# Performance work log

Hardware: AMD Instinct MI355X
Metric: run time of the kernel (lower is better)

Reference implementation:

```python
import jax, jax.numpy as jnp
import numpy as np

VP = 0.4
EP = 0.21

def _c_matrix():
    # Faithfully replicate the original Ci (including its asymmetric rows 2) and invert.
    Ci = np.zeros((6, 6), dtype=np.float64)
    Ci[0, 0] = 1 / EP; Ci[0, 1] = -VP / EP; Ci[0, 2] = -VP / EP
    Ci[1, 0] = -VP / EP; Ci[1, 1] = 1 / EP; Ci[1, 2] = -VP / EP
    Ci[2, 0] = -VP;      Ci[2, 1] = -VP;      Ci[2, 2] = 1 / EP
    Ci[3, 3] = 2 * (1 + VP) / EP
    Ci[4, 4] = 2 * (1 + VP) / EP
    Ci[5, 5] = 2 * (1 + VP) / EP
    return np.linalg.inv(Ci).astype(np.float32)

C_MAT = jnp.asarray(_c_matrix())
N = 12288

def setup_inputs() -> dict:
    key = jax.random.key(0)
    k1, k2, k3 = jax.random.split(key, 3)
    xyz = jax.random.normal(k1, (N, 3), dtype=jnp.float32)
    new_xyz = jax.random.normal(k2, (N, 3), dtype=jnp.float32)
    # ~half the points are 'inside' (gt_sdf < 1e-8)
    gt_sdf = jax.random.uniform(k3, (N,), dtype=jnp.float32) - 0.5
    return {"new_xyz": new_xyz, "xyz": xyz, "gt_sdf": gt_sdf}

def reference(new_xyz, xyz, gt_sdf):
    motion = new_xyz - xyz                      # [N,3]
    inside = gt_sdf < 1e-8                      # [N] bool, selects inside points
    w = new_xyz                                 # warped coordinates (KNN space)
    n = w.shape[0]
    # Brute-force NN among inside points (KDTree k=2, second neighbor == nearest non-self).
    sq = jnp.sum(w * w, axis=1)                 # [N]
    d2 = sq[:, None] + sq[None, :] - 2.0 * (w @ w.T)   # [N,N] squared distances
    BIG = jnp.float32(1e30)
    bad_col = (~inside)[None, :] | jnp.eye(n, dtype=bool)
    d2 = jnp.where(bad_col, BIG, d2)
    nn_idx = jnp.argmin(d2, axis=1)             # nearest inside neighbor (excluding self)
    nn_d = jnp.sqrt(jnp.maximum(jnp.min(d2, axis=1), 0.0))
    # tree_list1 filter: drop rows whose nearest neighbor is a duplicate point
    valid = inside & (nn_d > 1e-8)              # [N]
    dm = motion[nn_idx] - motion                # motion_delta
    dc = w[nn_idx] - w + 1e-8                   # cords_delta (+1e-8 as in original)
    v = valid[:, None]
    dm = jnp.where(v, dm, 0.0)                  # neutralize masked rows (keep shapes static)
    dc = jnp.where(v, dc, 1.0)
    du, dv, dw = dm[:, 0], dm[:, 1], dm[:, 2]
    dx, dy, dz = dc[:, 0], dc[:, 1], dc[:, 2]
    et = jnp.stack([du / dx, dv / dy, dw / dz,
                    (du / dy + dv / dx) / 2,
                    (du / dz + dw / dx) / 2,
                    (dw / dy + dv / dz) / 2], axis=1)   # [N,6] strain tensor
    # diag(et @ C @ et.T) as an O(N) batched quadratic form
    q = jnp.einsum('ni,ij,nj->n', et, C_MAT, et)
    q = jnp.where(valid, q, 0.0)
    n_valid = jnp.sum(valid).astype(jnp.float32)
    return jnp.linalg.norm(q) / n_valid
```

## Files before the change

### kernel.cpp

```cpp
#include <hip/hip_runtime.h>
#include <math.h>
#include <string.h>

#define N 12288
#define TILE 256
#define IB 512
#define NBX (N / IB)
#define NBY (N / TILE)

typedef unsigned long long ull;

struct CMat { float c[6][6]; };

template<int MODE>
__device__ __forceinline__ void nn_inner(
    const float4* __restrict__ tile, int tid,
    float wx0, float wy0, float wz0,
    float wx1, float wy1, float wz1,
    float& best0, int& bk0, float& best1, int& bk1)
{
    #pragma unroll 8
    for (int k = 0; k < TILE; ++k) {
        const float4 b = tile[k];
        const float d0 = fmaf(-2.0f, wx0 * b.x + wy0 * b.y + wz0 * b.z, b.w);
        const float d1 = fmaf(-2.0f, wx1 * b.x + wy1 * b.y + wz1 * b.z, b.w);
        bool ok0 = d0 < best0;
        bool ok1 = d1 < best1;
        if (MODE == 0) ok0 = ok0 && (k != tid);
        if (MODE == 1) ok1 = ok1 && (k != tid);
        if (ok0) { best0 = d0; bk0 = k; }
        if (ok1) { best1 = d1; bk1 = k; }
    }
}

__global__ __launch_bounds__(256) void nn_kernel(
    const float* __restrict__ new_xyz,
    const float* __restrict__ gt_sdf,
    ull* __restrict__ packed)
{
    const int tid = threadIdx.x;
    const int bx = blockIdx.x;
    const int by = blockIdx.y;

    const int i0 = bx * IB + tid;
    const int i1 = i0 + 256;

    const float wx0 = new_xyz[3 * i0 + 0];
    const float wy0 = new_xyz[3 * i0 + 1];
    const float wz0 = new_xyz[3 * i0 + 2];
    const float wx1 = new_xyz[3 * i1 + 0];
    const float wy1 = new_xyz[3 * i1 + 1];
    const float wz1 = new_xyz[3 * i1 + 2];

    __shared__ float4 tile[TILE];
    {
        const int j = by * TILE + tid;
        const float bxp = new_xyz[3 * j + 0];
        const float byp = new_xyz[3 * j + 1];
        const float bzp = new_xyz[3 * j + 2];
        const float sqj = bxp * bxp + byp * byp + bzp * bzp;
        const bool ins = gt_sdf[j] < 1e-8f;
        tile[tid] = make_float4(bxp, byp, bzp, ins ? sqj : 3e30f);
    }
    __syncthreads();

    float best0 = 3.0e38f, best1 = 3.0e38f;
    int bk0 = 0, bk1 = 0;

    if (by == 2 * bx)
        nn_inner<0>(tile, tid, wx0, wy0, wz0, wx1, wy1, wz1, best0, bk0, best1, bk1);
    else if (by == 2 * bx + 1)
        nn_inner<1>(tile, tid, wx0, wy0, wz0, wx1, wy1, wz1, best0, bk0, best1, bk1);
    else
        nn_inner<2>(tile, tid, wx0, wy0, wz0, wx1, wy1, wz1, best0, bk0, best1, bk1);

    const int jbase = by * TILE;

    unsigned kb0 = __float_as_uint(best0);
    kb0 = ((int)kb0 < 0) ? ~kb0 : (kb0 | 0x80000000u);
    packed[(size_t)by * N + i0] =
        ((ull)kb0 << 32) | (ull)(unsigned)(jbase + bk0);

    unsigned kb1 = __float_as_uint(best1);
    kb1 = ((int)kb1 < 0) ? ~kb1 : (kb1 | 0x80000000u);
    packed[(size_t)by * N + i1] =
        ((ull)kb1 << 32) | (ull)(unsigned)(jbase + bk1);
}

__global__ __launch_bounds__(256) void loss_kernel(
    const float* __restrict__ new_xyz,
    const float* __restrict__ xyz,
    const float* __restrict__ gt_sdf,
    const ull* __restrict__ packed,
    double* __restrict__ partial_sum,
    unsigned int* __restrict__ partial_cnt,
    CMat C)
{
    const int tid = threadIdx.x;
    const int i = blockIdx.x * 256 + tid;

    ull best = ~0ull;
    #pragma unroll
    for (int s = 0; s < NBY; ++s) {
        const ull p = packed[(size_t)s * N + i];
        best = (p < best) ? p : best;
    }

    const unsigned kb = (unsigned)(best >> 32);
    const unsigned bits = (kb & 0x80000000u) ? (kb ^ 0x80000000u) : ~kb;
    const float key = __uint_as_float(bits);
    const int nn = (int)(unsigned)(best & 0xffffffffu);

    const float wix = new_xyz[3 * i + 0];
    const float wiy = new_xyz[3 * i + 1];
    const float wiz = new_xyz[3 * i + 2];
    const float sqi = wix * wix + wiy * wiy + wiz * wiz;

    const float d2 = sqi + key;
    const float nnd = sqrtf(fmaxf(d2, 0.0f));
    const bool inside = gt_sdf[i] < 1e-8f;
    const bool valid = inside && (nnd > 1e-8f);

    float q = 0.0f;
    if (valid) {
        const float xix = xyz[3 * i + 0], xiy = xyz[3 * i + 1], xiz = xyz[3 * i + 2];
        const float wnx = new_xyz[3 * nn + 0], wny = new_xyz[3 * nn + 1], wnz = new_xyz[3 * nn + 2];
        const float xnx = xyz[3 * nn + 0],     xny = xyz[3 * nn + 1],     xnz = xyz[3 * nn + 2];

        const float du = (wnx - xnx) - (wix - xix);
        const float dv = (wny - xny) - (wiy - xiy);
        const float dw = (wnz - xnz) - (wiz - xiz);
        const float dx = wnx - wix + 1e-8f;
        const float dy = wny - wiy + 1e-8f;
        const float dz = wnz - wiz + 1e-8f;

        float et[6];
        et[0] = du / dx;
        et[1] = dv / dy;
        et[2] = dw / dz;
        et[3] = (du / dy + dv / dx) * 0.5f;
        et[4] = (du / dz + dw / dx) * 0.5f;
        et[5] = (dw / dy + dv / dz) * 0.5f;

        #pragma unroll
        for (int a = 0; a < 6; ++a) {
            float s = 0.0f;
            #pragma unroll
            for (int b = 0; b < 6; ++b) s += C.c[a][b] * et[b];
            q += et[a] * s;
        }
    }

    double q2 = (double)q * (double)q;
    #pragma unroll
    for (int off = 32; off > 0; off >>= 1)
        q2 += __shfl_down(q2, off, 64);
    const ull vm = __ballot(valid);
    const int lane = tid & 63;
    const int wid = tid >> 6;

    __shared__ double wsum[4];
    __shared__ unsigned wcnt[4];
    if (lane == 0) { wsum[wid] = q2; wcnt[wid] = (unsigned)__popcll(vm); }
    __syncthreads();
    if (tid == 0) {
        double s = wsum[0] + wsum[1] + wsum[2] + wsum[3];
        unsigned c = wcnt[0] + wcnt[1] + wcnt[2] + wcnt[3];
        partial_sum[blockIdx.x] = s;
        partial_cnt[blockIdx.x] = c;
    }
}

__global__ void final_kernel(const double* __restrict__ partial_sum,
                             const unsigned int* __restrict__ partial_cnt,
                             float* __restrict__ out)
{
    const int lane = threadIdx.x;
    double s = (lane < NBY) ? partial_sum[lane] : 0.0;
    double c = (lane < NBY) ? (double)partial_cnt[lane] : 0.0;
    #pragma unroll
    for (int off = 32; off > 0; off >>= 1) {
        s += __shfl_down(s, off, 64);
        c += __shfl_down(c, off, 64);
    }
    if (lane == 0) out[0] = (float)(sqrt(s) / c);
}

static void build_cmat(CMat* M)
{
    const double VP = 0.4, EP = 0.21;
    double A[6][12];
    memset(A, 0, sizeof(A));
    double Ci[6][6];
    memset(Ci, 0, sizeof(Ci));
    Ci[0][0] = 1.0 / EP; Ci[0][1] = -VP / EP; Ci[0][2] = -VP / EP;
    Ci[1][0] = -VP / EP; Ci[1][1] = 1.0 / EP; Ci[1][2] = -VP / EP;
    Ci[2][0] = -VP;      Ci[2][1] = -VP;      Ci[2][2] = 1.0 / EP;
    Ci[3][3] = 2.0 * (1.0 + VP) / EP;
    Ci[4][4] = Ci[3][3];
    Ci[5][5] = Ci[3][3];

    for (int i = 0; i < 6; ++i) {
        for (int j = 0; j < 6; ++j) A[i][j] = Ci[i][j];
        A[i][6 + i] = 1.0;
    }
    for (int col = 0; col < 6; ++col) {
        int piv = col;
        for (int r = col + 1; r < 6; ++r)
            if (fabs(A[r][col]) > fabs(A[piv][col])) piv = r;
        if (piv != col)
            for (int c = 0; c < 12; ++c) { double t = A[col][c]; A[col][c] = A[piv][c]; A[piv][c] = t; }
        const double d = A[col][col];
        for (int c = 0; c < 12; ++c) A[col][c] /= d;
        for (int r = 0; r < 6; ++r) {
            if (r == col) continue;
            const double f = A[r][col];
            if (f == 0.0) continue;
            for (int c = 0; c < 12; ++c) A[r][c] -= f * A[col][c];
        }
    }
    for (int i = 0; i < 6; ++i)
        for (int j = 0; j < 6; ++j)
            M->c[i][j] = (float)A[i][6 + j];
}

extern "C" void kernel_launch(void* const* d_in, const int* in_sizes, int n_in,
                              void* d_out, int out_size, void* d_ws, size_t ws_size,
                              hipStream_t stream)
{
    const float* new_xyz = (const float*)d_in[0];
    const float* xyz     = (const float*)d_in[1];
    const float* gt_sdf  = (const float*)d_in[2];
    float* out = (float*)d_out;

    const size_t packed_bytes = (size_t)NBY * N * sizeof(ull);
    ull* packed = (ull*)d_ws;
    double* partial_sum = (double*)((char*)d_ws + packed_bytes);
    unsigned int* partial_cnt = (unsigned int*)((char*)d_ws + packed_bytes + NBY * sizeof(double));

    CMat C;
    build_cmat(&C);

    nn_kernel<<<dim3(NBX, NBY), TILE, 0, stream>>>(new_xyz, gt_sdf, packed);
    loss_kernel<<<N / 256, 256, 0, stream>>>(new_xyz, xyz, gt_sdf, packed,
                                             partial_sum, partial_cnt, C);
    final_kernel<<<1, 64, 0, stream>>>(partial_sum, partial_cnt, out);
}
```

Measured before the change: 94.89 us.

## Register-block eight queries per thread with packed FP32 distance math

The nearest-neighbour kernel now holds eight query points per thread instead of two. Distances are computed with two-wide float vectors, so the compiler can emit packed FMA instructions, and the candidate tile shrinks to 96 points. Self-exclusion now checks index equality only in tiles that overlap the query range. The aim is to cut the shared-memory loads and instructions per pair. In exchange, the packed intermediate buffer grows to 128 partial rows per point, which means more global writes and a longer reduction in the loss kernel. The final reduction now uses a separate partial count, since that no longer matches the tile count.

```diff
diff --git a/kernel.cpp b/kernel.cpp
--- a/kernel.cpp
+++ b/kernel.cpp
@@ -3,33 +3,48 @@
 #include <string.h>
 
 #define N 12288
-#define TILE 256
-#define IB 512
+#define TILE 96
+#define ACCS 8
+#define IB (256 * ACCS)
 #define NBX (N / IB)
 #define NBY (N / TILE)
 
 typedef unsigned long long ull;
+typedef float v2f __attribute__((ext_vector_type(2)));
 
 struct CMat { float c[6][6]; };
 
-template<int MODE>
+__device__ __forceinline__ void upd(float dv, int k, bool excl,
+                                    float& bd, int& bk)
+{
+    if (!excl && dv < bd) { bd = dv; bk = k; }
+}
+
+template<bool CAREFUL>
 __device__ __forceinline__ void nn_inner(
-    const float4* __restrict__ tile, int tid,
-    float wx0, float wy0, float wz0,
-    float wx1, float wy1, float wz1,
-    float& best0, int& bk0, float& best1, int& bk1)
+    const float4* __restrict__ tile, int jbase, int ibase_t,
+    const v2f* wx, const v2f* wy, const v2f* wz,
+    float* bd, int* bk)
 {
     #pragma unroll 8
     for (int k = 0; k < TILE; ++k) {
         const float4 b = tile[k];
-        const float d0 = fmaf(-2.0f, wx0 * b.x + wy0 * b.y + wz0 * b.z, b.w);
-        const float d1 = fmaf(-2.0f, wx1 * b.x + wy1 * b.y + wz1 * b.z, b.w);
-        bool ok0 = d0 < best0;
-        bool ok1 = d1 < best1;
-        if (MODE == 0) ok0 = ok0 && (k != tid);
-        if (MODE == 1) ok1 = ok1 && (k != tid);
-        if (ok0) { best0 = d0; bk0 = k; }
-        if (ok1) { best1 = d1; bk1 = k; }
+        const int jj = jbase + k;
+        #pragma unroll
+        for (int g = 0; g < ACCS / 2; ++g) {
+            v2f dot = wx[g] * b.x;
+            dot = dot + wy[g] * b.y;
+            dot = dot + wz[g] * b.z;
+            const v2f d = b.w - 2.0f * dot;
+            const int a0 = 2 * g, a1 = 2 * g + 1;
+            bool e0 = false, e1 = false;
+            if (CAREFUL) {
+                e0 = (jj == ibase_t + a0 * 256);
+                e1 = (jj == ibase_t + a1 * 256);
+            }
+            upd(d.x, k, e0, bd[a0], bk[a0]);
+            upd(d.y, k, e1, bd[a1], bk[a1]);
+        }
     }
 }
 
@@ -42,49 +57,50 @@
     const int bx = blockIdx.x;
     const int by = blockIdx.y;
 
-    const int i0 = bx * IB + tid;
-    const int i1 = i0 + 256;
-
-    const float wx0 = new_xyz[3 * i0 + 0];
-    const float wy0 = new_xyz[3 * i0 + 1];
-    const float wz0 = new_xyz[3 * i0 + 2];
-    const float wx1 = new_xyz[3 * i1 + 0];
-    const float wy1 = new_xyz[3 * i1 + 1];
-    const float wz1 = new_xyz[3 * i1 + 2];
+    const int ibase = bx * IB;
+    const int ibase_t = ibase + tid;
+
+    v2f wx[ACCS / 2], wy[ACCS / 2], wz[ACCS / 2];
+    #pragma unroll
+    for (int g = 0; g < ACCS / 2; ++g) {
+        const int ia = ibase_t + (2 * g) * 256;
+        const int ib2 = ibase_t + (2 * g + 1) * 256;
+        wx[g] = (v2f){ new_xyz[3 * ia + 0], new_xyz[3 * ib2 + 0] };
+        wy[g] = (v2f){ new_xyz[3 * ia + 1], new_xyz[3 * ib2 + 1] };
+        wz[g] = (v2f){ new_xyz[3 * ia + 2], new_xyz[3 * ib2 + 2] };
+    }
 
     __shared__ float4 tile[TILE];
-    {
-        const int j = by * TILE + tid;
-        const float bxp = new_xyz[3 * j + 0];
-        const float byp = new_xyz[3 * j + 1];
-        const float bzp = new_xyz[3 * j + 2];
-        const float sqj = bxp * bxp + byp * byp + bzp * bzp;
+    const int jbase = by * TILE;
+    if (tid < TILE) {
+        const int j = jbase + tid;
+        const float px = new_xyz[3 * j + 0];
+        const float py = new_xyz[3 * j + 1];
+        const float pz = new_xyz[3 * j + 2];
+        const float sqj = px * px + py * py + pz * pz;
         const bool ins = gt_sdf[j] < 1e-8f;
-        tile[tid] = make_float4(bxp, byp, bzp, ins ? sqj : 3e30f);
+        tile[tid] = make_float4(px, py, pz, ins ? sqj : 3e30f);
     }
     __syncthreads();
 
-    float best0 = 3.0e38f, best1 = 3.0e38f;
-    int bk0 = 0, bk1 = 0;
-
-    if (by == 2 * bx)
-        nn_inner<0>(tile, tid, wx0, wy0, wz0, wx1, wy1, wz1, best0, bk0, best1, bk1);
-    else if (by == 2 * bx + 1)
-        nn_inner<1>(tile, tid, wx0, wy0, wz0, wx1, wy1, wz1, best0, bk0, best1, bk1);
+    float bd[ACCS];
+    int bk[ACCS];
+    #pragma unroll
+    for (int a = 0; a < ACCS; ++a) { bd[a] = 3.0e38f; bk[a] = 0; }
+
+    const bool dirty = (jbase < ibase + IB) && (jbase + TILE > ibase);
+    if (dirty)
+        nn_inner<true>(tile, jbase, ibase_t, wx, wy, wz, bd, bk);
     else
-        nn_inner<2>(tile, tid, wx0, wy0, wz0, wx1, wy1, wz1, best0, bk0, best1, bk1);
-
-    const int jbase = by * TILE;
-
-    unsigned kb0 = __float_as_uint(best0);
-    kb0 = ((int)kb0 < 0) ? ~kb0 : (kb0 | 0x80000000u);
-    packed[(size_t)by * N + i0] =
-        ((ull)kb0 << 32) | (ull)(unsigned)(jbase + bk0);
-
-    unsigned kb1 = __float_as_uint(best1);
-    kb1 = ((int)kb1 < 0) ? ~kb1 : (kb1 | 0x80000000u);
-    packed[(size_t)by * N + i1] =
-        ((ull)kb1 << 32) | (ull)(unsigned)(jbase + bk1);
+        nn_inner<false>(tile, jbase, ibase_t, wx, wy, wz, bd, bk);
+
+    #pragma unroll
+    for (int a = 0; a < ACCS; ++a) {
+        unsigned kb = __float_as_uint(bd[a]);
+        kb = ((int)kb < 0) ? ~kb : (kb | 0x80000000u);
+        packed[(size_t)by * N + (ibase_t + a * 256)] =
+            ((ull)kb << 32) | (ull)(unsigned)(jbase + bk[a]);
+    }
 }
 
 __global__ __launch_bounds__(256) void loss_kernel(
@@ -100,7 +116,7 @@
     const int i = blockIdx.x * 256 + tid;
 
     ull best = ~0ull;
-    #pragma unroll
+    #pragma unroll 8
     for (int s = 0; s < NBY; ++s) {
         const ull p = packed[(size_t)s * N + i];
         best = (p < best) ? p : best;
@@ -171,13 +187,15 @@
     }
 }
 
+#define NPART (N / 256)
+
 __global__ void final_kernel(const double* __restrict__ partial_sum,
                              const unsigned int* __restrict__ partial_cnt,
                              float* __restrict__ out)
 {
     const int lane = threadIdx.x;
-    double s = (lane < NBY) ? partial_sum[lane] : 0.0;
-    double c = (lane < NBY) ? (double)partial_cnt[lane] : 0.0;
+    double s = (lane < NPART) ? partial_sum[lane] : 0.0;
+    double c = (lane < NPART) ? (double)partial_cnt[lane] : 0.0;
     #pragma unroll
     for (int off = 32; off > 0; off >>= 1) {
         s += __shfl_down(s, off, 64);
@@ -236,12 +254,13 @@
     const size_t packed_bytes = (size_t)NBY * N * sizeof(ull);
     ull* packed = (ull*)d_ws;
     double* partial_sum = (double*)((char*)d_ws + packed_bytes);
-    unsigned int* partial_cnt = (unsigned int*)((char*)d_ws + packed_bytes + NBY * sizeof(double));
+    unsigned int* partial_cnt =
+        (unsigned int*)((char*)d_ws + packed_bytes + NPART * sizeof(double));
 
     CMat C;
     build_cmat(&C);
 
-    nn_kernel<<<dim3(NBX, NBY), TILE, 0, stream>>>(new_xyz, gt_sdf, packed);
+    nn_kernel<<<dim3(NBX, NBY), 256, 0, stream>>>(new_xyz, gt_sdf, packed);
     loss_kernel<<<N / 256, 256, 0, stream>>>(new_xyz, xyz, gt_sdf, packed,
                                              partial_sum, partial_cnt, C);
     final_kernel<<<1, 64, 0, stream>>>(partial_sum, partial_cnt, out);
```

Result: slower. 104.4 us (+10.0%).
